# Optimization experiments

Measured on AMD Instinct MI355X. Metric: run time of the kernel, lower is better.

## Reference

```python
import jax, jax.numpy as jnp
import numpy as np

NUM_HEADS = 12
HEAD_DIM = 32
GP_NUM = 20


def setup_inputs() -> dict:
    key = jax.random.key(0)
    k1, k2, k3, k4 = jax.random.split(key, 4)
    B, H, W, C = 4, 32, 32, 384
    att = NUM_HEADS * HEAD_DIM  # == C (required by single group_mode)
    x = jax.random.normal(k1, (B, H, W, C), dtype=jnp.float32)
    W_qkv = jax.random.normal(k2, (3 * att, C), dtype=jnp.float32) * (C ** -0.5)
    W_proj = jax.random.normal(k3, (C, att), dtype=jnp.float32) * (att ** -0.5)
    W_gp = jax.random.normal(k4, (GP_NUM, C), dtype=jnp.float32) * (C ** -0.5)
    return {"x": x, "W_qkv": W_qkv, "W_proj": W_proj, "W_gp": W_gp}


def reference(x, W_qkv, W_proj, W_gp):
    B, H, W_, C = x.shape
    N = H * W_
    h, d = NUM_HEADS, HEAD_DIM
    scale = d ** -0.5

    qkv = x.reshape(B, N, C) @ W_qkv.T                      # [B,N,3hd]
    q, k, v = jnp.split(qkv, 3, axis=-1)
    q = q.reshape(B, N, h, d).transpose(0, 2, 1, 3)          # [B,h,N,d]
    k = k.reshape(B, N, h, d).transpose(0, 2, 1, 3)
    v = v.reshape(B, N, h, d).transpose(0, 2, 1, 3)

    attn = jax.nn.softmax(jnp.einsum('bhnd,bhmd->bhnm', q, k) * scale, axis=-1)

    # single group mode: hard top-1 group assignment from all-head q
    q_all = q.transpose(0, 2, 1, 3).reshape(B, N, h * d)     # [B,N,hd]
    gw = q_all @ W_gp.T                                      # [B,N,GP_NUM]
    oh = jax.nn.one_hot(jnp.argmax(gw, axis=-1), GP_NUM, dtype=attn.dtype)
    G = jnp.einsum('bng,bmg->bnm', oh, oh)                   # [B,N,N] same-group mask
    Gh = jnp.concatenate([
        jnp.broadcast_to(G[:, None], (B, h // 2, N, N)),
        jnp.broadcast_to(1.0 - G[:, None], (B, h // 2, N, N)),
    ], axis=1)                                               # [B,h,N,N]

    attn = attn * Gh
    # unusual column-wise renorm: sum over query axis (dim=2)
    attn = attn / (attn.sum(axis=2, keepdims=True) + 1e-8)

    out = jnp.einsum('bhnm,bhmd->bhnd', attn, v)
    out = out.transpose(0, 2, 1, 3).reshape(B, H, W_, h * d)
    return out @ W_proj.T
```

## Files before the change

### kernel.cpp

```cpp
#include <hip/hip_runtime.h>
#include <hip/hip_bf16.h>


#define B_    4
#define N_    1024
#define C_    384
#define H3_   1152
#define NH_   12
#define HD_   32
#define GP_   20
#define BH_   48
#define SCALE 0.17677669529663687f

typedef __attribute__((ext_vector_type(8))) short bf16x8;
typedef __attribute__((ext_vector_type(4))) float f32x4;

static __device__ __forceinline__ unsigned short f2bf(float x) {
  union { float f; unsigned u; } v; v.f = x;
  unsigned r = v.u + 0x7fff + ((v.u >> 16) & 1);
  return (unsigned short)(r >> 16);
}
static __device__ __forceinline__ float bf2f(unsigned short h) {
  union { unsigned u; float f; } v; v.u = ((unsigned)h) << 16;
  return v.f;
}

__global__ __launch_bounds__(256) void conv3(const float* __restrict__ x,
                                             const float* __restrict__ wq,
                                             const float* __restrict__ wp,
                                             unsigned short* __restrict__ xh,
                                             unsigned short* __restrict__ xl,
                                             unsigned short* __restrict__ wqh,
                                             unsigned short* __restrict__ wql,
                                             unsigned short* __restrict__ wph,
                                             unsigned short* __restrict__ wpl) {
  const int NX = (4096 * C_) / 4, NQ = (H3_ * C_) / 4, NP = (C_ * C_) / 4;
  int idx = blockIdx.x * 256 + threadIdx.x;
  const float* src; unsigned short *dh, *dl; int o;
  if (idx < NX)            { src = x;  dh = xh;  dl = xl;  o = idx; }
  else if (idx < NX + NQ)  { src = wq; dh = wqh; dl = wql; o = idx - NX; }
  else if (idx < NX + NQ + NP) { src = wp; dh = wph; dl = wpl; o = idx - NX - NQ; }
  else return;
  float4 v = *(const float4*)(src + (size_t)o * 4);
  float a[4] = {v.x, v.y, v.z, v.w};
  unsigned short h[4], lo[4];
  #pragma unroll
  for (int i = 0; i < 4; ++i) { h[i] = f2bf(a[i]); lo[i] = f2bf(a[i] - bf2f(h[i])); }
  uint2 ph = {(unsigned)h[0]  | ((unsigned)h[1]  << 16),
              (unsigned)h[2]  | ((unsigned)h[3]  << 16)};
  uint2 pl = {(unsigned)lo[0] | ((unsigned)lo[1] << 16),
              (unsigned)lo[2] | ((unsigned)lo[3] << 16)};
  *(uint2*)(dh + (size_t)o * 4) = ph;
  *(uint2*)(dl + (size_t)o * 4) = pl;
}

__global__ __launch_bounds__(256) void wgp_fuse(const float* __restrict__ Wqkv,
                                                const float* __restrict__ Wgp,
                                                double* __restrict__ M) {
  int idx = blockIdx.x * 256 + threadIdx.x;
  if (idx >= GP_ * C_) return;
  int g = idx / C_, c = idx % C_;
  double acc = 0.0;
  for (int j = 0; j < C_; ++j)
    acc += (double)Wgp[g * C_ + j] * (double)Wqkv[(size_t)j * C_ + c];
  M[idx] = acc;
}

__global__ __launch_bounds__(320) void group_assign2(const float* __restrict__ x,
                                                     const double* __restrict__ M,
                                                     int* __restrict__ group) {
  __shared__ double sc[16][GP_];
  int tid = threadIdx.x;
  int r = tid / GP_, g = tid % GP_;
  int n = blockIdx.x * 16 + r;
  const float* row = x + (size_t)n * C_;
  const double* w = M + (size_t)g * C_;
  double acc = 0.0;
  for (int c = 0; c < C_; ++c) acc += (double)row[c] * w[c];
  sc[r][g] = acc;
  __syncthreads();
  if (g == 0) {
    int best = 0; double bv = sc[r][0];
    #pragma unroll
    for (int j = 1; j < GP_; ++j)
      if (sc[r][j] > bv) { bv = sc[r][j]; best = j; }
    group[n] = best;
  }
}

template<int MODE>
__global__ __launch_bounds__(256) void gemm_mfma(
    const unsigned short* __restrict__ Ah_g, const unsigned short* __restrict__ Al_g,
    const unsigned short* __restrict__ Bh_g, const unsigned short* __restrict__ Bl_g,
    float* __restrict__ Cm, int Nn,
    unsigned short* __restrict__ Qh, unsigned short* __restrict__ Ql,
    unsigned short* __restrict__ Kh, unsigned short* __restrict__ Kl,
    float* __restrict__ Vf) {
  __shared__ __align__(16) unsigned short sAh[128 * 40];
  __shared__ __align__(16) unsigned short sAl[128 * 40];
  __shared__ __align__(16) unsigned short sBh[128 * 40];
  __shared__ __align__(16) unsigned short sBl[128 * 40];
  int tid = threadIdx.x;
  int l = tid & 63, w = tid >> 6;
  int lanelo = l & 15, g16 = l >> 4;
  int wr = w >> 1, wc = w & 1;
  int bn = blockIdx.x, bm = blockIdx.y;

  const unsigned short* sg;
  unsigned short* sd;
  int rb;
  if (w == 0)      { sg = Ah_g; sd = sAh; rb = bm; }
  else if (w == 1) { sg = Al_g; sd = sAl; rb = bm; }
  else if (w == 2) { sg = Bh_g; sd = sBh; rb = bn; }
  else             { sg = Bl_g; sd = sBl; rb = bn; }
  const unsigned short* gsrc = sg + (size_t)(rb * 128 + (l >> 2)) * C_ + (l & 3) * 8;
  unsigned short* ldst = sd + (l >> 2) * 40 + (l & 3) * 8;

  f32x4 acc[4][4];
  #pragma unroll
  for (int i = 0; i < 4; ++i)
    #pragma unroll
    for (int j = 0; j < 4; ++j) acc[i][j] = (f32x4){0.f, 0.f, 0.f, 0.f};

  for (int kk = 0; kk < C_; kk += 32) {
    __syncthreads();
    #pragma unroll
    for (int i = 0; i < 8; ++i) {
      uint4 v = *(const uint4*)(gsrc + (size_t)(i * 16) * C_ + kk);
      *(uint4*)(ldst + i * 16 * 40) = v;
    }
    __syncthreads();
    bf16x8 ah[4], al[4], bh8[4], bl8[4];
    #pragma unroll
    for (int i = 0; i < 4; ++i) {
      int r = (wr * 64 + i * 16 + lanelo) * 40 + g16 * 8;
      ah[i] = *(const bf16x8*)(sAh + r);
      al[i] = *(const bf16x8*)(sAl + r);
    }
    #pragma unroll
    for (int j = 0; j < 4; ++j) {
      int r = (wc * 64 + j * 16 + lanelo) * 40 + g16 * 8;
      bh8[j] = *(const bf16x8*)(sBh + r);
      bl8[j] = *(const bf16x8*)(sBl + r);
    }
    #pragma unroll
    for (int i = 0; i < 4; ++i)
      #pragma unroll
      for (int j = 0; j < 4; ++j) {
        acc[i][j] = __builtin_amdgcn_mfma_f32_16x16x32_bf16(ah[i], bh8[j], acc[i][j], 0, 0, 0);
        acc[i][j] = __builtin_amdgcn_mfma_f32_16x16x32_bf16(ah[i], bl8[j], acc[i][j], 0, 0, 0);
        acc[i][j] = __builtin_amdgcn_mfma_f32_16x16x32_bf16(al[i], bh8[j], acc[i][j], 0, 0, 0);
      }
  }

  if (MODE == 0) {
    #pragma unroll
    for (int i = 0; i < 4; ++i) {
      int mm = bm * 128 + wr * 64 + i * 16 + g16 * 4;
      #pragma unroll
      for (int j = 0; j < 4; ++j) {
        int c = bn * 128 + wc * 64 + j * 16 + lanelo;
        #pragma unroll
        for (int t = 0; t < 4; ++t)
          Cm[(size_t)(mm + t) * Nn + c] = acc[i][j][t];
      }
    }
  } else {
    int region = bn / 3;
    #pragma unroll
    for (int i = 0; i < 4; ++i) {
      int mm0 = bm * 128 + wr * 64 + i * 16 + g16 * 4;
      #pragma unroll
      for (int j = 0; j < 4; ++j) {
        int c = bn * 128 + wc * 64 + j * 16 + lanelo;
        int cc = c - region * 384;
        #pragma unroll
        for (int t = 0; t < 4; ++t) {
          int mm = mm0 + t;
          int b = mm >> 10, n = mm & 1023;
          float v = acc[i][j][t];
          if (region == 0) {
            v *= SCALE;
            unsigned short h = f2bf(v), lo = f2bf(v - bf2f(h));
            size_t idx = ((size_t)(b * NH_ + (cc >> 5)) * N_ + n) * HD_ + (cc & 31);
            Qh[idx] = h; Ql[idx] = lo;
          } else if (region == 1) {
            unsigned short h = f2bf(v), lo = f2bf(v - bf2f(h));
            size_t idx = ((size_t)(b * NH_ + (cc >> 5)) * N_ + n) * HD_ + (cc & 31);
            Kh[idx] = h; Kl[idx] = lo;
          } else {
            Vf[(size_t)mm * C_ + cc] = v;
          }
        }
      }
    }
  }
}

__global__ __launch_bounds__(256) void score(const unsigned short* __restrict__ Qh,
                                             const unsigned short* __restrict__ Ql,
                                             const unsigned short* __restrict__ Kh,
                                             const unsigned short* __restrict__ Kl,
                                             const int* __restrict__ group,
                                             float* __restrict__ rinv,
                                             unsigned short* __restrict__ Pp) {
  __shared__ __align__(16) unsigned short kbufh[4096];
  __shared__ __align__(16) unsigned short kbufl[4096];
  __shared__ __align__(16) float bounce[4][256];
  __shared__ int g_s[1024];
  int tid = threadIdx.x;
  int l = tid & 63, w = tid >> 6;
  int lanelo = l & 15, g16 = l >> 4;
  int flat = blockIdx.y * 16 + blockIdx.x;
  int nf = (flat & 7) * 96 + (flat >> 3);
  int bh = nf >> 4, blk = nf & 15;
  int b = bh / NH_;
  bool samehead = ((bh % NH_) < NH_ / 2);
  int q0 = blk * 64 + w * 16;
  size_t bhb = (size_t)bh * (N_ * HD_);

  *(int4*)&g_s[tid * 4] = *(const int4*)(group + b * N_ + tid * 4);
  bf16x8 aQh = *(const bf16x8*)(Qh + bhb + (size_t)(q0 + lanelo) * HD_ + g16 * 8);
  bf16x8 aQl = *(const bf16x8*)(Ql + bhb + (size_t)(q0 + lanelo) * HD_ + g16 * 8);
  __syncthreads();
  int gq[4];
  #pragma unroll
  for (int t = 0; t < 4; ++t) gq[t] = g_s[q0 + g16 * 4 + t];

  float s4[4] = {0.f, 0.f, 0.f, 0.f};
  size_t pbase = (size_t)bh * 64 * 1024 * 16;

  for (int ch = 0; ch < 8; ++ch) {
    __syncthreads();
    #pragma unroll
    for (int t2 = 0; t2 < 2; ++t2) {
      int f2 = t2 * 256 + tid;
      int row = f2 >> 2, c4 = f2 & 3;
      uint4 vh = *(const uint4*)(Kh + bhb + (size_t)(ch * 128 + row) * HD_ + c4 * 8);
      uint4 vl = *(const uint4*)(Kl + bhb + (size_t)(ch * 128 + row) * HD_ + c4 * 8);
      int phys = row * 64 + ((c4 ^ (row & 3)) << 4);
      *(uint4*)((char*)kbufh + phys) = vh;
      *(uint4*)((char*)kbufl + phys) = vl;
    }
    __syncthreads();
    #pragma unroll
    for (int kt2 = 0; kt2 < 8; ++kt2) {
      int kt = ch * 8 + kt2;
      int kvl = kt2 * 16 + lanelo;
      int phys = kvl * 64 + ((g16 ^ (kvl & 3)) << 4);
      bf16x8 bh8 = *(const bf16x8*)((char*)kbufh + phys);
      bf16x8 bl8 = *(const bf16x8*)((char*)kbufl + phys);
      f32x4 acc = {0.f, 0.f, 0.f, 0.f};
      acc = __builtin_amdgcn_mfma_f32_16x16x32_bf16(aQh, bh8, acc, 0, 0, 0);
      acc = __builtin_amdgcn_mfma_f32_16x16x32_bf16(aQh, bl8, acc, 0, 0, 0);
      acc = __builtin_amdgcn_mfma_f32_16x16x32_bf16(aQl, bh8, acc, 0, 0, 0);
      int gcol = g_s[kt * 16 + lanelo];
      #pragma unroll
      for (int t = 0; t < 4; ++t) {
        float e = __expf(acc[t]);
        s4[t] += e;
        int r = g16 * 4 + t;
        bool keep = ((gcol == gq[t]) == samehead);
        float me = keep ? e : 0.f;
        int pc = (lanelo >> 2) ^ (r & 3) ^ (r >> 2);
        bounce[w][r * 16 + pc * 4 + (lanelo & 3)] = me;
      }
      int r2 = l >> 2;
      int pc2 = (l & 3) ^ (r2 & 3) ^ (r2 >> 2);
      float4 pv4 = *(float4*)&bounce[w][r2 * 16 + pc2 * 4];
      unsigned u0 = ((unsigned)f2bf(pv4.y) << 16) | f2bf(pv4.x);
      unsigned u1 = ((unsigned)f2bf(pv4.w) << 16) | f2bf(pv4.z);
      uint2 st = {u0, u1};
      *(uint2*)(Pp + pbase + ((size_t)kt * 1024 + q0 + r2) * 16 + (l & 3) * 4) = st;
    }
  }
  #pragma unroll
  for (int t = 0; t < 4; ++t) {
    #pragma unroll
    for (int off = 1; off < 16; off <<= 1) s4[t] += __shfl_xor(s4[t], off);
  }
  if (lanelo == 0) {
    #pragma unroll
    for (int t = 0; t < 4; ++t)
      rinv[(size_t)bh * N_ + q0 + g16 * 4 + t] = 1.0f / s4[t];
  }
}

__global__ __launch_bounds__(256) void colpass(const unsigned short* __restrict__ Pp,
                                               const float* __restrict__ rinv,
                                               const float* __restrict__ Vf,
                                               unsigned short* __restrict__ Vth,
                                               unsigned short* __restrict__ Vtl) {
  __shared__ float red[256][9];
  __shared__ float colinv_s[16];
  __shared__ unsigned short vh_s[32][16];
  __shared__ unsigned short vl_s[32][16];
  int tid = threadIdx.x;
  int flat = blockIdx.y * 64 + blockIdx.x;
  int nf = (flat & 7) * 384 + (flat >> 3);
  int bh = nf >> 6, mt = nf & 63;
  int b = bh / NH_, hd = bh % NH_;
  const unsigned short* pb = Pp + ((size_t)(bh * 64 + mt) * 1024) * 16;
  const float* rv = rinv + (size_t)bh * N_;
  int oct = tid & 1, nrow0 = tid >> 1;
  float s[8] = {};
  #pragma unroll
  for (int p = 0; p < 8; ++p) {
    int n = p * 128 + nrow0;
    uint4 v = *(const uint4*)(pb + (size_t)n * 16 + oct * 8);
    float rn = rv[n];
    s[0] += bf2f((unsigned short)(v.x & 0xffff)) * rn;
    s[1] += bf2f((unsigned short)(v.x >> 16)) * rn;
    s[2] += bf2f((unsigned short)(v.y & 0xffff)) * rn;
    s[3] += bf2f((unsigned short)(v.y >> 16)) * rn;
    s[4] += bf2f((unsigned short)(v.z & 0xffff)) * rn;
    s[5] += bf2f((unsigned short)(v.z >> 16)) * rn;
    s[6] += bf2f((unsigned short)(v.w & 0xffff)) * rn;
    s[7] += bf2f((unsigned short)(v.w >> 16)) * rn;
  }
  int ridx = oct * 128 + nrow0;
  #pragma unroll
  for (int j = 0; j < 8; ++j) red[ridx][j] = s[j];
  __syncthreads();
  for (int st = 64; st > 0; st >>= 1) {
    if (nrow0 < st) {
      #pragma unroll
      for (int j = 0; j < 8; ++j) red[ridx][j] += red[ridx + st][j];
    }
    __syncthreads();
  }
  if (tid < 16)
    colinv_s[tid] = 1.0f / (red[(tid >> 3) * 128][tid & 7] + 1e-8f);
  __syncthreads();
  if (tid < 128) {
    int m = tid >> 3, d4 = (tid & 7) * 4;
    float4 v = *(const float4*)(Vf + ((size_t)(b * N_ + mt * 16 + m)) * C_ +
                                hd * HD_ + d4);
    float ci = colinv_s[m];
    float va[4] = {v.x * ci, v.y * ci, v.z * ci, v.w * ci};
    #pragma unroll
    for (int i = 0; i < 4; ++i) {
      unsigned short h = f2bf(va[i]);
      vh_s[d4 + i][m] = h;
      vl_s[d4 + i][m] = f2bf(va[i] - bf2f(h));
    }
  }
  __syncthreads();
  if (tid < 64) {
    int d = tid >> 1, m8 = (tid & 1) * 8;
    uint4 h = *(uint4*)&vh_s[d][m8];
    *(uint4*)(Vth + ((size_t)bh * HD_ + d) * N_ + mt * 16 + m8) = h;
  } else if (tid < 128) {
    int t2 = tid - 64;
    int d = t2 >> 1, m8 = (t2 & 1) * 8;
    uint4 lo = *(uint4*)&vl_s[d][m8];
    *(uint4*)(Vtl + ((size_t)bh * HD_ + d) * N_ + mt * 16 + m8) = lo;
  }
}

__global__ __launch_bounds__(256) void pv(const unsigned short* __restrict__ Pp,
                                          const unsigned short* __restrict__ Vth,
                                          const unsigned short* __restrict__ Vtl,
                                          const float* __restrict__ rinv,
                                          unsigned short* __restrict__ aoh,
                                          unsigned short* __restrict__ aol) {
  int tid = threadIdx.x;
  int l = tid & 63, w = tid >> 6;
  int lanelo = l & 15, g16 = l >> 4;
  int flat = blockIdx.y * 8 + blockIdx.x;
  int nf = (flat & 7) * 48 + (flat >> 3);
  int bh = nf >> 3, nt = nf & 7;
  int b = bh / NH_, hd = bh % NH_;
  int n0 = nt * 128 + w * 32;
  size_t pB = (size_t)bh * 64 * 1024 * 16;
  const unsigned short* vh = Vth + (size_t)bh * HD_ * N_;
  const unsigned short* vl = Vtl + (size_t)bh * HD_ * N_;
  f32x4 o00 = {0.f,0.f,0.f,0.f}, o01 = {0.f,0.f,0.f,0.f};
  f32x4 o10 = {0.f,0.f,0.f,0.f}, o11 = {0.f,0.f,0.f,0.f};
  for (int kc = 0; kc < 32; ++kc) {
    int mt = kc * 2 + (g16 >> 1);
    int mi = (g16 & 1) * 8;
    bf16x8 a0 = *(const bf16x8*)(Pp + pB + ((size_t)mt * 1024 + n0 + lanelo) * 16 + mi);
    bf16x8 a1 = *(const bf16x8*)(Pp + pB + ((size_t)mt * 1024 + n0 + 16 + lanelo) * 16 + mi);
    size_t vo0 = (size_t)lanelo * N_ + kc * 32 + g16 * 8;
    size_t vo1 = (size_t)(16 + lanelo) * N_ + kc * 32 + g16 * 8;
    bf16x8 b0h = *(const bf16x8*)(vh + vo0);
    bf16x8 b0l = *(const bf16x8*)(vl + vo0);
    bf16x8 b1h = *(const bf16x8*)(vh + vo1);
    bf16x8 b1l = *(const bf16x8*)(vl + vo1);
    o00 = __builtin_amdgcn_mfma_f32_16x16x32_bf16(a0, b0h, o00, 0, 0, 0);
    o00 = __builtin_amdgcn_mfma_f32_16x16x32_bf16(a0, b0l, o00, 0, 0, 0);
    o01 = __builtin_amdgcn_mfma_f32_16x16x32_bf16(a0, b1h, o01, 0, 0, 0);
    o01 = __builtin_amdgcn_mfma_f32_16x16x32_bf16(a0, b1l, o01, 0, 0, 0);
    o10 = __builtin_amdgcn_mfma_f32_16x16x32_bf16(a1, b0h, o10, 0, 0, 0);
    o10 = __builtin_amdgcn_mfma_f32_16x16x32_bf16(a1, b0l, o10, 0, 0, 0);
    o11 = __builtin_amdgcn_mfma_f32_16x16x32_bf16(a1, b1h, o11, 0, 0, 0);
    o11 = __builtin_amdgcn_mfma_f32_16x16x32_bf16(a1, b1l, o11, 0, 0, 0);
  }
  float4 rv0 = *(const float4*)(rinv + (size_t)bh * N_ + n0 + g16 * 4);
  float4 rv1 = *(const float4*)(rinv + (size_t)bh * N_ + n0 + 16 + g16 * 4);
  float r0a[4] = {rv0.x, rv0.y, rv0.z, rv0.w};
  float r1a[4] = {rv1.x, rv1.y, rv1.z, rv1.w};
  #pragma unroll
  for (int t = 0; t < 4; ++t) {
    size_t row0 = (size_t)(b * N_ + n0 + g16 * 4 + t) * C_ + hd * HD_;
    size_t row1 = (size_t)(b * N_ + n0 + 16 + g16 * 4 + t) * C_ + hd * HD_;
    float v00 = o00[t] * r0a[t], v01 = o01[t] * r0a[t];
    float v10 = o10[t] * r1a[t], v11 = o11[t] * r1a[t];
    unsigned short h;
    h = f2bf(v00); aoh[row0 + lanelo]      = h; aol[row0 + lanelo]      = f2bf(v00 - bf2f(h));
    h = f2bf(v01); aoh[row0 + 16 + lanelo] = h; aol[row0 + 16 + lanelo] = f2bf(v01 - bf2f(h));
    h = f2bf(v10); aoh[row1 + lanelo]      = h; aol[row1 + lanelo]      = f2bf(v10 - bf2f(h));
    h = f2bf(v11); aoh[row1 + 16 + lanelo] = h; aol[row1 + 16 + lanelo] = f2bf(v11 - bf2f(h));
  }
}

extern "C" void kernel_launch(void* const* d_in, const int* in_sizes, int n_in,
                              void* d_out, int out_size, void* d_ws, size_t ws_size,
                              hipStream_t stream) {
  const float* x     = (const float*)d_in[0];
  const float* Wqkv  = (const float*)d_in[1];
  const float* Wproj = (const float*)d_in[2];
  const float* Wgp   = (const float*)d_in[3];
  float* out = (float*)d_out;

  char* base = (char*)d_ws;
  size_t off = 0;
  auto alloc = [&](size_t bytes) {
    void* p = base + off;
    off += (bytes + 255) & ~(size_t)255;
    return p;
  };
  float*  Vf    = (float*)alloc(4096ull * C_ * 4);
  float*  rinv  = (float*)alloc((size_t)BH_ * N_ * 4);
  double* Mgp   = (double*)alloc((size_t)GP_ * C_ * 8);
  int*    group = (int*)alloc(4096ull * 4);
  unsigned short* xh  = (unsigned short*)alloc(4096ull * C_ * 2);
  unsigned short* xl  = (unsigned short*)alloc(4096ull * C_ * 2);
  unsigned short* Wqh = (unsigned short*)alloc((size_t)H3_ * C_ * 2);
  unsigned short* Wql = (unsigned short*)alloc((size_t)H3_ * C_ * 2);
  unsigned short* Wph = (unsigned short*)alloc((size_t)C_ * C_ * 2);
  unsigned short* Wpl = (unsigned short*)alloc((size_t)C_ * C_ * 2);
  unsigned short* aoh = (unsigned short*)alloc(4096ull * C_ * 2);
  unsigned short* aol = (unsigned short*)alloc(4096ull * C_ * 2);
  const size_t BSZ = (size_t)BH_ * N_ * HD_;
  unsigned short* Qh  = (unsigned short*)alloc(BSZ * 2);
  unsigned short* Ql  = (unsigned short*)alloc(BSZ * 2);
  unsigned short* Kh  = (unsigned short*)alloc(BSZ * 2);
  unsigned short* Kl  = (unsigned short*)alloc(BSZ * 2);
  unsigned short* Vth = (unsigned short*)alloc(BSZ * 2);
  unsigned short* Vtl = (unsigned short*)alloc(BSZ * 2);
  unsigned short* Pp  = (unsigned short*)alloc((size_t)BH_ * N_ * N_ * 2);

  conv3<<<dim3(2112), 256, 0, stream>>>(x, Wqkv, Wproj, xh, xl, Wqh, Wql, Wph, Wpl);
  wgp_fuse<<<dim3(30), 256, 0, stream>>>(Wqkv, Wgp, Mgp);
  group_assign2<<<dim3(256), 320, 0, stream>>>(x, Mgp, group);
  gemm_mfma<1><<<dim3(9, 32), 256, 0, stream>>>(xh, xl, Wqh, Wql, nullptr, H3_,
                                                Qh, Ql, Kh, Kl, Vf);
  score<<<dim3(16, BH_), 256, 0, stream>>>(Qh, Ql, Kh, Kl, group, rinv, Pp);
  colpass<<<dim3(64, BH_), 256, 0, stream>>>(Pp, rinv, Vf, Vth, Vtl);
  pv<<<dim3(8, BH_), 256, 0, stream>>>(Pp, Vth, Vtl, rinv, aoh, aol);
  gemm_mfma<0><<<dim3(3, 32), 256, 0, stream>>>(aoh, aol, Wph, Wpl, out, C_,
                                                nullptr, nullptr, nullptr, nullptr, nullptr);
}
```

Baseline: 191.8 us.

## Shrink GEMM tiles to 64x64, prefetch next K slice, swizzle block order

The split-bf16 MFMA GEMMs (QKV projection and output projection) now use 64x64 output tiles instead of 128x128. This raises the grid from 288 and 96 blocks to 1152 and 384, so more of the GPU's compute units get work. The next K slice is loaded into registers while the current one is computed, giving a simple register double-buffer. A flat grid with an XCD-style swizzle of the block index is meant to improve cache locality. Smaller tiles lower data reuse per block and add total global and LDS traffic.

New measurement: 244.3 us. +27.4%, slower.

```diff
diff --git a/kernel.cpp b/kernel.cpp
--- a/kernel.cpp
+++ b/kernel.cpp
@@ -89,22 +89,24 @@
 }
 
 template<int MODE>
-__global__ __launch_bounds__(256) void gemm_mfma(
+__global__ __launch_bounds__(256) void gemm_mfma64(
     const unsigned short* __restrict__ Ah_g, const unsigned short* __restrict__ Al_g,
     const unsigned short* __restrict__ Bh_g, const unsigned short* __restrict__ Bl_g,
-    float* __restrict__ Cm, int Nn,
+    float* __restrict__ Cm, int Nn, int nbn, int nwg8,
     unsigned short* __restrict__ Qh, unsigned short* __restrict__ Ql,
     unsigned short* __restrict__ Kh, unsigned short* __restrict__ Kl,
     float* __restrict__ Vf) {
-  __shared__ __align__(16) unsigned short sAh[128 * 40];
-  __shared__ __align__(16) unsigned short sAl[128 * 40];
-  __shared__ __align__(16) unsigned short sBh[128 * 40];
-  __shared__ __align__(16) unsigned short sBl[128 * 40];
+  __shared__ __align__(16) unsigned short sAh[64 * 40];
+  __shared__ __align__(16) unsigned short sAl[64 * 40];
+  __shared__ __align__(16) unsigned short sBh[64 * 40];
+  __shared__ __align__(16) unsigned short sBl[64 * 40];
   int tid = threadIdx.x;
   int l = tid & 63, w = tid >> 6;
   int lanelo = l & 15, g16 = l >> 4;
   int wr = w >> 1, wc = w & 1;
-  int bn = blockIdx.x, bm = blockIdx.y;
+  int flat = blockIdx.x;
+  int swz = (flat & 7) * nwg8 + (flat >> 3);
+  int bm = swz / nbn, bn = swz % nbn;
 
   const unsigned short* sg;
   unsigned short* sd;
@@ -113,40 +115,48 @@
   else if (w == 1) { sg = Al_g; sd = sAl; rb = bm; }
   else if (w == 2) { sg = Bh_g; sd = sBh; rb = bn; }
   else             { sg = Bl_g; sd = sBl; rb = bn; }
-  const unsigned short* gsrc = sg + (size_t)(rb * 128 + (l >> 2)) * C_ + (l & 3) * 8;
+  const unsigned short* gsrc = sg + (size_t)(rb * 64 + (l >> 2)) * C_ + (l & 3) * 8;
   unsigned short* ldst = sd + (l >> 2) * 40 + (l & 3) * 8;
 
-  f32x4 acc[4][4];
+  uint4 r[4];
   #pragma unroll
   for (int i = 0; i < 4; ++i)
-    #pragma unroll
-    for (int j = 0; j < 4; ++j) acc[i][j] = (f32x4){0.f, 0.f, 0.f, 0.f};
-
-  for (int kk = 0; kk < C_; kk += 32) {
+    r[i] = *(const uint4*)(gsrc + (size_t)(i * 16) * C_);
+
+  f32x4 acc[2][2];
+  #pragma unroll
+  for (int i = 0; i < 2; ++i)
+    #pragma unroll
+    for (int j = 0; j < 2; ++j) acc[i][j] = (f32x4){0.f, 0.f, 0.f, 0.f};
+
+  for (int kk = 0; kk < 12; ++kk) {
+    if (kk) __syncthreads();
+    #pragma unroll
+    for (int i = 0; i < 4; ++i)
+      *(uint4*)(ldst + i * 16 * 40) = r[i];
     __syncthreads();
-    #pragma unroll
-    for (int i = 0; i < 8; ++i) {
-      uint4 v = *(const uint4*)(gsrc + (size_t)(i * 16) * C_ + kk);
-      *(uint4*)(ldst + i * 16 * 40) = v;
-    }
-    __syncthreads();
-    bf16x8 ah[4], al[4], bh8[4], bl8[4];
-    #pragma unroll
-    for (int i = 0; i < 4; ++i) {
-      int r = (wr * 64 + i * 16 + lanelo) * 40 + g16 * 8;
-      ah[i] = *(const bf16x8*)(sAh + r);
-      al[i] = *(const bf16x8*)(sAl + r);
-    }
-    #pragma unroll
-    for (int j = 0; j < 4; ++j) {
-      int r = (wc * 64 + j * 16 + lanelo) * 40 + g16 * 8;
-      bh8[j] = *(const bf16x8*)(sBh + r);
-      bl8[j] = *(const bf16x8*)(sBl + r);
-    }
-    #pragma unroll
-    for (int i = 0; i < 4; ++i)
-      #pragma unroll
-      for (int j = 0; j < 4; ++j) {
+    if (kk < 11) {
+      #pragma unroll
+      for (int i = 0; i < 4; ++i)
+        r[i] = *(const uint4*)(gsrc + (size_t)(i * 16) * C_ + (kk + 1) * 32);
+    }
+    bf16x8 ah[2], al[2], bh8[2], bl8[2];
+    #pragma unroll
+    for (int i = 0; i < 2; ++i) {
+      int rr = (wr * 32 + i * 16 + lanelo) * 40 + g16 * 8;
+      ah[i] = *(const bf16x8*)(sAh + rr);
+      al[i] = *(const bf16x8*)(sAl + rr);
+    }
+    #pragma unroll
+    for (int j = 0; j < 2; ++j) {
+      int rr = (wc * 32 + j * 16 + lanelo) * 40 + g16 * 8;
+      bh8[j] = *(const bf16x8*)(sBh + rr);
+      bl8[j] = *(const bf16x8*)(sBl + rr);
+    }
+    #pragma unroll
+    for (int i = 0; i < 2; ++i)
+      #pragma unroll
+      for (int j = 0; j < 2; ++j) {
         acc[i][j] = __builtin_amdgcn_mfma_f32_16x16x32_bf16(ah[i], bh8[j], acc[i][j], 0, 0, 0);
         acc[i][j] = __builtin_amdgcn_mfma_f32_16x16x32_bf16(ah[i], bl8[j], acc[i][j], 0, 0, 0);
         acc[i][j] = __builtin_amdgcn_mfma_f32_16x16x32_bf16(al[i], bh8[j], acc[i][j], 0, 0, 0);
@@ -155,24 +165,24 @@
 
   if (MODE == 0) {
     #pragma unroll
-    for (int i = 0; i < 4; ++i) {
-      int mm = bm * 128 + wr * 64 + i * 16 + g16 * 4;
-      #pragma unroll
-      for (int j = 0; j < 4; ++j) {
-        int c = bn * 128 + wc * 64 + j * 16 + lanelo;
+    for (int i = 0; i < 2; ++i) {
+      int mm = bm * 64 + wr * 32 + i * 16 + g16 * 4;
+      #pragma unroll
+      for (int j = 0; j < 2; ++j) {
+        int c = bn * 64 + wc * 32 + j * 16 + lanelo;
         #pragma unroll
         for (int t = 0; t < 4; ++t)
           Cm[(size_t)(mm + t) * Nn + c] = acc[i][j][t];
       }
     }
   } else {
-    int region = bn / 3;
-    #pragma unroll
-    for (int i = 0; i < 4; ++i) {
-      int mm0 = bm * 128 + wr * 64 + i * 16 + g16 * 4;
-      #pragma unroll
-      for (int j = 0; j < 4; ++j) {
-        int c = bn * 128 + wc * 64 + j * 16 + lanelo;
+    int region = bn / 6;
+    #pragma unroll
+    for (int i = 0; i < 2; ++i) {
+      int mm0 = bm * 64 + wr * 32 + i * 16 + g16 * 4;
+      #pragma unroll
+      for (int j = 0; j < 2; ++j) {
+        int c = bn * 64 + wc * 32 + j * 16 + lanelo;
         int cc = c - region * 384;
         #pragma unroll
         for (int t = 0; t < 4; ++t) {
@@ -455,11 +465,13 @@
   conv3<<<dim3(2112), 256, 0, stream>>>(x, Wqkv, Wproj, xh, xl, Wqh, Wql, Wph, Wpl);
   wgp_fuse<<<dim3(30), 256, 0, stream>>>(Wqkv, Wgp, Mgp);
   group_assign2<<<dim3(256), 320, 0, stream>>>(x, Mgp, group);
-  gemm_mfma<1><<<dim3(9, 32), 256, 0, stream>>>(xh, xl, Wqh, Wql, nullptr, H3_,
-                                                Qh, Ql, Kh, Kl, Vf);
+  gemm_mfma64<1><<<dim3(1152), 256, 0, stream>>>(xh, xl, Wqh, Wql, nullptr,
+                                                 H3_, 18, 144,
+                                                 Qh, Ql, Kh, Kl, Vf);
   score<<<dim3(16, BH_), 256, 0, stream>>>(Qh, Ql, Kh, Kl, group, rinv, Pp);
   colpass<<<dim3(64, BH_), 256, 0, stream>>>(Pp, rinv, Vf, Vth, Vtl);
   pv<<<dim3(8, BH_), 256, 0, stream>>>(Pp, Vth, Vtl, rinv, aoh, aol);
-  gemm_mfma<0><<<dim3(3, 32), 256, 0, stream>>>(aoh, aol, Wph, Wpl, out, C_,
+  gemm_mfma64<0><<<dim3(384), 256, 0, stream>>>(aoh, aol, Wph, Wpl, out,
+                                                C_, 6, 48,
                                                 nullptr, nullptr, nullptr, nullptr, nullptr);
 }
```
